# Optimization experiments

Measured on AMD Instinct MI355X. Metric: run time of the kernel, lower is better.

Reference implementation:

```python
import jax, jax.numpy as jnp
import numpy as np

N_NODES = 100000
N_EDGES = 3200000
IN_F, HID, OUT = 3, 32, 1
NEG_SLOPE = 0.2


def _glorot(key, shape):
    fan_in, fan_out = shape[0], shape[-1]
    lim = jnp.sqrt(6.0 / (fan_in + fan_out)).astype(jnp.float32)
    return jax.random.uniform(key, shape, jnp.float32, -lim, lim)


def setup_inputs() -> dict:
    key = jax.random.key(0)
    ks = jax.random.split(key, 12)
    x = jax.random.normal(ks[0], (N_NODES, IN_F), jnp.float32)
    edge_index = jax.random.randint(ks[1], (2, N_EDGES), 0, N_NODES, jnp.int32)
    return {
        "x": x,
        "edge_index": edge_index,
        "W1": _glorot(ks[2], (IN_F, HID)),
        "att_src1": _glorot(ks[3], (1, HID))[0],
        "att_dst1": _glorot(ks[4], (1, HID))[0],
        "b1": jnp.zeros((HID,), jnp.float32),
        "W2": _glorot(ks[5], (HID, HID)),
        "att_src2": _glorot(ks[6], (1, HID))[0],
        "att_dst2": _glorot(ks[7], (1, HID))[0],
        "b2": jnp.zeros((HID,), jnp.float32),
        "Wl": _glorot(ks[8], (HID, OUT)),
        "bl": jnp.zeros((OUT,), jnp.float32),
    }


def gat_layer(x, src, dst, W, att_src, att_dst, b):
    # h: [N, HID] dense transform
    h = x @ W
    # per-node attention halves (compute once per node, gather per edge)
    a_s = h @ att_src  # [N]
    a_d = h @ att_dst  # [N]
    logits = jax.nn.leaky_relu(a_s[src] + a_d[dst], NEG_SLOPE)  # [E+N]
    # segment-softmax over incoming edges of each dst node
    m = jax.ops.segment_max(logits, dst, num_segments=N_NODES)
    m = jnp.where(jnp.isfinite(m), m, 0.0)
    ex = jnp.exp(logits - m[dst])
    denom = jax.ops.segment_sum(ex, dst, num_segments=N_NODES)
    coef = ex / (denom[dst] + 1e-16)
    # weighted scatter-aggregate of source messages
    out = jax.ops.segment_sum(coef[:, None] * h[src], dst, num_segments=N_NODES)
    return out + b


def reference(x, edge_index, W1, att_src1, att_dst1, b1, W2, att_src2, att_dst2, b2, Wl, bl):
    # PyG GATConv default: add self-loops
    loops = jnp.arange(N_NODES, dtype=edge_index.dtype)
    src = jnp.concatenate([edge_index[0], loops])
    dst = jnp.concatenate([edge_index[1], loops])
    h = gat_layer(x, src, dst, W1, att_src1, att_dst1, b1)
    h = jax.nn.relu(h)  # dropout is identity in eval
    h = gat_layer(h, src, dst, W2, att_src2, att_dst2, b2)
    h = jax.nn.relu(h)
    return h @ Wl + bl
```

## Files before the change

### kernel.cpp

```cpp
#include <hip/hip_runtime.h>
#include <hip/hip_fp16.h>

#define HID 32
#define BN 132
#define NBPAD 768
#define BSTRIDE 5120
#define CHUNK 4096

__device__ __forceinline__ float lrelu(float x) { return x > 0.0f ? x : 0.2f * x; }

__global__ void k_transform1(const float* __restrict__ x,
                             const float* __restrict__ W1,
                             const float* __restrict__ att_src,
                             const float* __restrict__ att_dst,
                             __half* __restrict__ hh,
                             float* __restrict__ a_s,
                             float* __restrict__ a_d,
                             int* __restrict__ cursor,
                             int N)
{
    int tid = blockIdx.x * blockDim.x + threadIdx.x;
    if (tid < NBPAD) cursor[tid] = 0;
    int n = tid >> 5;
    int f = tid & 31;
    if (n >= N) return;
    float x0 = x[n * 3 + 0], x1 = x[n * 3 + 1], x2 = x[n * 3 + 2];
    float hv = x0 * W1[f] + x1 * W1[HID + f] + x2 * W1[2 * HID + f];
    hh[(size_t)n * HID + f] = __float2half(hv);
    float as = hv * att_src[f];
    float ad = hv * att_dst[f];
    #pragma unroll
    for (int m = 16; m >= 1; m >>= 1) {
        as += __shfl_xor(as, m, 32);
        ad += __shfl_xor(ad, m, 32);
    }
    if (f == 0) { a_s[n] = as; a_d[n] = ad; }
}

__global__ void __launch_bounds__(256) k_binscatter(const int* __restrict__ src,
                                                    const int* __restrict__ dst,
                                                    int* __restrict__ cursor,
                                                    unsigned int* __restrict__ packed,
                                                    int NBr, int E)
{
    __shared__ int stage[CHUNK];
    __shared__ unsigned short sbid[CHUNK];
    __shared__ int lhist[NBPAD], lexcl[NBPAD], lbase[NBPAD], lcur[NBPAD];
    __shared__ int arr[256];
    int t = threadIdx.x;
    for (int i = t; i < NBPAD; i += 256) { lhist[i] = 0; lcur[i] = 0; }
    __syncthreads();
    int base = blockIdx.x * CHUNK;
    int cnt = E - base; if (cnt > CHUNK) cnt = CHUNK;
    for (int i = t; i < cnt; i += 256)
        atomicAdd(&lhist[dst[base + i] / BN], 1);
    __syncthreads();
    int b0 = 3 * t;
    int c0 = lhist[b0], c1 = lhist[b0 + 1], c2 = lhist[b0 + 2];
    int s = c0 + c1 + c2;
    arr[t] = s;
    __syncthreads();
    for (int o = 1; o < 256; o <<= 1) {
        int v = (t >= o) ? arr[t - o] : 0;
        __syncthreads();
        arr[t] += v;
        __syncthreads();
    }
    int ex = arr[t] - s;
    int e0 = ex, e1 = ex + c0, e2 = ex + c0 + c1;
    lexcl[b0] = e0; lexcl[b0 + 1] = e1; lexcl[b0 + 2] = e2;
    for (int i = 0; i < c0; ++i) sbid[e0 + i] = (unsigned short)b0;
    for (int i = 0; i < c1; ++i) sbid[e1 + i] = (unsigned short)(b0 + 1);
    for (int i = 0; i < c2; ++i) sbid[e2 + i] = (unsigned short)(b0 + 2);
    for (int b = t; b < NBr; b += 256)
        if (lhist[b]) lbase[b] = b * BSTRIDE + atomicAdd(&cursor[b], lhist[b]);
    __syncthreads();
    for (int i = t; i < cnt; i += 256) {
        int d = dst[base + i];
        int sv = src[base + i];
        int b = d / BN;
        int dl = d - b * BN;
        int idx = lexcl[b] + atomicAdd(&lcur[b], 1);
        stage[idx] = (int)((unsigned)sv | ((unsigned)dl << 17));
    }
    __syncthreads();
    for (int i = t; i < cnt; i += 256) {
        int b = sbid[i];
        int gpos = lbase[b] + (i - lexcl[b]);
        if (gpos < (b + 1) * BSTRIDE)
            packed[gpos] = (unsigned)stage[i];
    }
}

__device__ __forceinline__ void agg_node(const __half* __restrict__ hh,
                                         const float* __restrict__ a_s,
                                         float a_dn, float a_sn,
                                         const float* __restrict__ b,
                                         int n, int f,
                                         const int* lcsr, int off, int dg,
                                         float& vx, float& vy)
{
    float ex = __expf(lrelu(a_sn + a_dn));
    float den = ex;
    float2 hs = __half22float2(*(const __half2*)(hh + (size_t)n * HID + 2 * f));
    float accx = ex * hs.x;
    float accy = ex * hs.y;
    for (int base = 0; base < dg; base += 16) {
        int m = dg - base; if (m > 16) m = 16;
        int sv = 0;
        float exv = 0.0f;
        if (f < m) {
            sv = lcsr[off + base + f];
            exv = __expf(lrelu(a_s[sv] + a_dn));
        }
        int j = 0;
        for (; j + 8 <= m; j += 8) {
            int s0 = __shfl(sv, j, 16), s1 = __shfl(sv, j + 1, 16);
            int s2 = __shfl(sv, j + 2, 16), s3 = __shfl(sv, j + 3, 16);
            int s4 = __shfl(sv, j + 4, 16), s5 = __shfl(sv, j + 5, 16);
            int s6 = __shfl(sv, j + 6, 16), s7 = __shfl(sv, j + 7, 16);
            float e0 = __shfl(exv, j, 16), e1 = __shfl(exv, j + 1, 16);
            float e2 = __shfl(exv, j + 2, 16), e3 = __shfl(exv, j + 3, 16);
            float e4 = __shfl(exv, j + 4, 16), e5 = __shfl(exv, j + 5, 16);
            float e6 = __shfl(exv, j + 6, 16), e7 = __shfl(exv, j + 7, 16);
            __half2 p0 = *(const __half2*)(hh + (size_t)s0 * HID + 2 * f);
            __half2 p1 = *(const __half2*)(hh + (size_t)s1 * HID + 2 * f);
            __half2 p2 = *(const __half2*)(hh + (size_t)s2 * HID + 2 * f);
            __half2 p3 = *(const __half2*)(hh + (size_t)s3 * HID + 2 * f);
            __half2 p4 = *(const __half2*)(hh + (size_t)s4 * HID + 2 * f);
            __half2 p5 = *(const __half2*)(hh + (size_t)s5 * HID + 2 * f);
            __half2 p6 = *(const __half2*)(hh + (size_t)s6 * HID + 2 * f);
            __half2 p7 = *(const __half2*)(hh + (size_t)s7 * HID + 2 * f);
            float2 q0 = __half22float2(p0), q1 = __half22float2(p1);
            float2 q2 = __half22float2(p2), q3 = __half22float2(p3);
            float2 q4 = __half22float2(p4), q5 = __half22float2(p5);
            float2 q6 = __half22float2(p6), q7 = __half22float2(p7);
            den += ((e0 + e1) + (e2 + e3)) + ((e4 + e5) + (e6 + e7));
            accx = fmaf(e0, q0.x, accx); accy = fmaf(e0, q0.y, accy);
            accx = fmaf(e1, q1.x, accx); accy = fmaf(e1, q1.y, accy);
            accx = fmaf(e2, q2.x, accx); accy = fmaf(e2, q2.y, accy);
            accx = fmaf(e3, q3.x, accx); accy = fmaf(e3, q3.y, accy);
            accx = fmaf(e4, q4.x, accx); accy = fmaf(e4, q4.y, accy);
            accx = fmaf(e5, q5.x, accx); accy = fmaf(e5, q5.y, accy);
            accx = fmaf(e6, q6.x, accx); accy = fmaf(e6, q6.y, accy);
            accx = fmaf(e7, q7.x, accx); accy = fmaf(e7, q7.y, accy);
        }
        for (; j + 4 <= m; j += 4) {
            int s0 = __shfl(sv, j, 16), s1 = __shfl(sv, j + 1, 16);
            int s2 = __shfl(sv, j + 2, 16), s3 = __shfl(sv, j + 3, 16);
            float e0 = __shfl(exv, j, 16), e1 = __shfl(exv, j + 1, 16);
            float e2 = __shfl(exv, j + 2, 16), e3 = __shfl(exv, j + 3, 16);
            __half2 p0 = *(const __half2*)(hh + (size_t)s0 * HID + 2 * f);
            __half2 p1 = *(const __half2*)(hh + (size_t)s1 * HID + 2 * f);
            __half2 p2 = *(const __half2*)(hh + (size_t)s2 * HID + 2 * f);
            __half2 p3 = *(const __half2*)(hh + (size_t)s3 * HID + 2 * f);
            float2 q0 = __half22float2(p0), q1 = __half22float2(p1);
            float2 q2 = __half22float2(p2), q3 = __half22float2(p3);
            den += (e0 + e1) + (e2 + e3);
            accx = fmaf(e0, q0.x, accx); accy = fmaf(e0, q0.y, accy);
            accx = fmaf(e1, q1.x, accx); accy = fmaf(e1, q1.y, accy);
            accx = fmaf(e2, q2.x, accx); accy = fmaf(e2, q2.y, accy);
            accx = fmaf(e3, q3.x, accx); accy = fmaf(e3, q3.y, accy);
        }
        for (; j < m; ++j) {
            int s0 = __shfl(sv, j, 16);
            float e0 = __shfl(exv, j, 16);
            float2 q0 = __half22float2(*(const __half2*)(hh + (size_t)s0 * HID + 2 * f));
            den += e0;
            accx = fmaf(e0, q0.x, accx);
            accy = fmaf(e0, q0.y, accy);
        }
    }
    float inv = 1.0f / (den + 1e-16f);
    vx = fmaxf(accx * inv + b[2 * f], 0.0f);
    vy = fmaxf(accy * inv + b[2 * f + 1], 0.0f);
}

__device__ __forceinline__ int build_lcsr(const unsigned int* pk, int cnt,
                                          int* lcsr, int* lhist, int* lscan, int* lcur)
{
    int t = threadIdx.x;
    if (t < 256) { lhist[t] = 0; lcur[t] = 0; }
    __syncthreads();
    for (int i = t; i < cnt; i += 512)
        atomicAdd(&lhist[(pk[i] >> 17) & 255], 1);
    __syncthreads();
    if (t < 256) lscan[t] = lhist[t];
    __syncthreads();
    for (int o = 1; o < 256; o <<= 1) {
        int v = (t < 256 && t >= o) ? lscan[t - o] : 0;
        __syncthreads();
        if (t < 256) lscan[t] += v;
        __syncthreads();
    }
    for (int i = t; i < cnt; i += 512) {
        unsigned int p = pk[i];
        int dl = (p >> 17) & 255;
        int pos = atomicAdd(&lcur[dl], 1);
        lcsr[(lscan[dl] - lhist[dl]) + pos] = (int)(p & 0x1FFFF);
    }
    __syncthreads();
    return cnt;
}

__global__ void __launch_bounds__(512) k_agg_mid_f(const __half* __restrict__ hh,
                          const float* __restrict__ a_s,
                          const float* __restrict__ a_d,
                          const int* __restrict__ cursor,
                          const unsigned int* __restrict__ packed,
                          const float* __restrict__ b1,
                          const float* __restrict__ W2,
                          const float* __restrict__ as2w,
                          const float* __restrict__ ad2w,
                          __half* __restrict__ hh_out,
                          float* __restrict__ as_out,
                          float* __restrict__ ad_out,
                          int N)
{
    __shared__ int lcsr[BSTRIDE];
    __shared__ int lhist[256], lscan[256], lcur[256];
    int bk = blockIdx.x, t = threadIdx.x;
    int cnt = cursor[bk]; if (cnt > BSTRIDE) cnt = BSTRIDE;
    build_lcsr(packed + (size_t)bk * BSTRIDE, cnt, lcsr, lhist, lscan, lcur);
    int g = t >> 4, f = t & 15;
    for (int dl = g; dl < BN; dl += 32) {
        int n = bk * BN + dl;
        if (n >= N) continue;
        int off = lscan[dl] - lhist[dl];
        int dg = lhist[dl];
        float vx, vy;
        agg_node(hh, a_s, a_d[n], a_s[n], b1, n, f, lcsr, off, dg, vx, vy);
        float hx = 0.0f, hy = 0.0f;
        #pragma unroll
        for (int k = 0; k < 16; ++k) {
            float va = __shfl(vx, k, 16);
            float vb = __shfl(vy, k, 16);
            float2 w0 = *(const float2*)(W2 + (2 * k) * HID + 2 * f);
            float2 w1 = *(const float2*)(W2 + (2 * k + 1) * HID + 2 * f);
            hx = fmaf(va, w0.x, hx); hy = fmaf(va, w0.y, hy);
            hx = fmaf(vb, w1.x, hx); hy = fmaf(vb, w1.y, hy);
        }
        *(__half2*)(hh_out + (size_t)n * HID + 2 * f) = __floats2half2_rn(hx, hy);
        float as = hx * as2w[2 * f] + hy * as2w[2 * f + 1];
        float ad = hx * ad2w[2 * f] + hy * ad2w[2 * f + 1];
        #pragma unroll
        for (int m2 = 8; m2 >= 1; m2 >>= 1) {
            as += __shfl_xor(as, m2, 16);
            ad += __shfl_xor(ad, m2, 16);
        }
        if (f == 0) { as_out[n] = as; ad_out[n] = ad; }
    }
}

__global__ void __launch_bounds__(512) k_agg_out_f(const __half* __restrict__ hh,
                          const float* __restrict__ a_s,
                          const float* __restrict__ a_d,
                          const int* __restrict__ cursor,
                          const unsigned int* __restrict__ packed,
                          const float* __restrict__ b2,
                          const float* __restrict__ Wl,
                          const float* __restrict__ bl,
                          float* __restrict__ out,
                          int N)
{
    __shared__ int lcsr[BSTRIDE];
    __shared__ int lhist[256], lscan[256], lcur[256];
    int bk = blockIdx.x, t = threadIdx.x;
    int cnt = cursor[bk]; if (cnt > BSTRIDE) cnt = BSTRIDE;
    build_lcsr(packed + (size_t)bk * BSTRIDE, cnt, lcsr, lhist, lscan, lcur);
    int g = t >> 4, f = t & 15;
    for (int dl = g; dl < BN; dl += 32) {
        int n = bk * BN + dl;
        if (n >= N) continue;
        int off = lscan[dl] - lhist[dl];
        int dg = lhist[dl];
        float vx, vy;
        agg_node(hh, a_s, a_d[n], a_s[n], b2, n, f, lcsr, off, dg, vx, vy);
        float y = vx * Wl[2 * f] + vy * Wl[2 * f + 1];
        #pragma unroll
        for (int m2 = 8; m2 >= 1; m2 >>= 1)
            y += __shfl_xor(y, m2, 16);
        if (f == 0) out[n] = y + bl[0];
    }
}

extern "C" void kernel_launch(void* const* d_in, const int* in_sizes, int n_in,
                              void* d_out, int out_size, void* d_ws, size_t ws_size,
                              hipStream_t stream)
{
    const float* x        = (const float*)d_in[0];
    const int*   eidx     = (const int*)d_in[1];
    const float* W1       = (const float*)d_in[2];
    const float* att_src1 = (const float*)d_in[3];
    const float* att_dst1 = (const float*)d_in[4];
    const float* b1       = (const float*)d_in[5];
    const float* W2       = (const float*)d_in[6];
    const float* att_src2 = (const float*)d_in[7];
    const float* att_dst2 = (const float*)d_in[8];
    const float* b2       = (const float*)d_in[9];
    const float* Wl       = (const float*)d_in[10];
    const float* bl       = (const float*)d_in[11];
    float* out = (float*)d_out;

    int N = in_sizes[0] / 3;
    int E = in_sizes[1] / 2;
    const int* src = eidx;
    const int* dst = eidx + E;
    int NBr = (N + BN - 1) / BN;

    size_t szNHh = (size_t)N * HID * 2;
    size_t szN4  = (size_t)N * 4;
    size_t szPK  = (size_t)NBr * BSTRIDE * 4;

    char* ws = (char*)d_ws;
    __half* h1h    = (__half*)ws; ws += szNHh;
    __half* h2h    = (__half*)ws; ws += szNHh;
    unsigned int* packed = (unsigned int*)ws; ws += szPK;
    float*  a_s1   = (float*)ws;  ws += szN4;
    float*  a_d1   = (float*)ws;  ws += szN4;
    float*  a_s2   = (float*)ws;  ws += szN4;
    float*  a_d2   = (float*)ws;  ws += szN4;
    int*    cursor = (int*)ws;    ws += NBPAD * 4;

    const int B = 256;
    int gridNode32 = (N * HID + B - 1) / B;
    int gridBin    = (E + CHUNK - 1) / CHUNK;

    k_transform1<<<gridNode32, B, 0, stream>>>(x, W1, att_src1, att_dst1,
                                               h1h, a_s1, a_d1, cursor, N);
    k_binscatter<<<gridBin, B, 0, stream>>>(src, dst, cursor, packed, NBr, E);
    k_agg_mid_f<<<NBr, 512, 0, stream>>>(h1h, a_s1, a_d1, cursor, packed,
                                         b1, W2, att_src2, att_dst2,
                                         h2h, a_s2, a_d2, N);
    k_agg_out_f<<<NBr, 512, 0, stream>>>(h2h, a_s2, a_d2, cursor, packed,
                                         b2, Wl, bl, out, N);
}
```

Baseline: 259.7 us.

## Aggregate each node with 8 lanes of 4 features using 8-byte gathers

The per-node aggregation group shrinks from 16 lanes handling 2 half features each to 8 lanes handling 4 features each. Each gather becomes an 8-byte load, and two nodes are processed per 16 lanes. Edges are consumed in batches of 8, with all loads issued before the FMAs. The W2 transform and reductions are reshaped to match. This aims to halve the gather instruction count and improve lane utilisation for low-degree nodes, at the cost of more registers and fewer edges batched per shuffle round.

```diff
diff --git a/kernel.cpp b/kernel.cpp
--- a/kernel.cpp
+++ b/kernel.cpp
@@ -92,92 +92,72 @@
     }
 }
 
-__device__ __forceinline__ void agg_node(const __half* __restrict__ hh,
-                                         const float* __restrict__ a_s,
-                                         float a_dn, float a_sn,
-                                         const float* __restrict__ b,
-                                         int n, int f,
-                                         const int* lcsr, int off, int dg,
-                                         float& vx, float& vy)
+__device__ __forceinline__ void agg_node8(const __half* __restrict__ hh,
+                                          const float* __restrict__ a_s,
+                                          float a_dn, float a_sn,
+                                          const float* __restrict__ b,
+                                          int n, int f,
+                                          const int* lcsr, int off, int dg,
+                                          float& v0, float& v1, float& v2, float& v3)
 {
     float ex = __expf(lrelu(a_sn + a_dn));
     float den = ex;
-    float2 hs = __half22float2(*(const __half2*)(hh + (size_t)n * HID + 2 * f));
-    float accx = ex * hs.x;
-    float accy = ex * hs.y;
-    for (int base = 0; base < dg; base += 16) {
-        int m = dg - base; if (m > 16) m = 16;
+    float2 sr = *(const float2*)(hh + (size_t)n * HID + 4 * f);
+    float2 s01 = __half22float2(*(__half2*)&sr.x);
+    float2 s23 = __half22float2(*(__half2*)&sr.y);
+    float a0 = ex * s01.x, a1 = ex * s01.y, a2 = ex * s23.x, a3 = ex * s23.y;
+    for (int base = 0; base < dg; base += 8) {
+        int m = dg - base; if (m > 8) m = 8;
         int sv = 0;
         float exv = 0.0f;
         if (f < m) {
             sv = lcsr[off + base + f];
             exv = __expf(lrelu(a_s[sv] + a_dn));
         }
-        int j = 0;
-        for (; j + 8 <= m; j += 8) {
-            int s0 = __shfl(sv, j, 16), s1 = __shfl(sv, j + 1, 16);
-            int s2 = __shfl(sv, j + 2, 16), s3 = __shfl(sv, j + 3, 16);
-            int s4 = __shfl(sv, j + 4, 16), s5 = __shfl(sv, j + 5, 16);
-            int s6 = __shfl(sv, j + 6, 16), s7 = __shfl(sv, j + 7, 16);
-            float e0 = __shfl(exv, j, 16), e1 = __shfl(exv, j + 1, 16);
-            float e2 = __shfl(exv, j + 2, 16), e3 = __shfl(exv, j + 3, 16);
-            float e4 = __shfl(exv, j + 4, 16), e5 = __shfl(exv, j + 5, 16);
-            float e6 = __shfl(exv, j + 6, 16), e7 = __shfl(exv, j + 7, 16);
-            __half2 p0 = *(const __half2*)(hh + (size_t)s0 * HID + 2 * f);
-            __half2 p1 = *(const __half2*)(hh + (size_t)s1 * HID + 2 * f);
-            __half2 p2 = *(const __half2*)(hh + (size_t)s2 * HID + 2 * f);
-            __half2 p3 = *(const __half2*)(hh + (size_t)s3 * HID + 2 * f);
-            __half2 p4 = *(const __half2*)(hh + (size_t)s4 * HID + 2 * f);
-            __half2 p5 = *(const __half2*)(hh + (size_t)s5 * HID + 2 * f);
-            __half2 p6 = *(const __half2*)(hh + (size_t)s6 * HID + 2 * f);
-            __half2 p7 = *(const __half2*)(hh + (size_t)s7 * HID + 2 * f);
-            float2 q0 = __half22float2(p0), q1 = __half22float2(p1);
-            float2 q2 = __half22float2(p2), q3 = __half22float2(p3);
-            float2 q4 = __half22float2(p4), q5 = __half22float2(p5);
-            float2 q6 = __half22float2(p6), q7 = __half22float2(p7);
-            den += ((e0 + e1) + (e2 + e3)) + ((e4 + e5) + (e6 + e7));
-            accx = fmaf(e0, q0.x, accx); accy = fmaf(e0, q0.y, accy);
-            accx = fmaf(e1, q1.x, accx); accy = fmaf(e1, q1.y, accy);
-            accx = fmaf(e2, q2.x, accx); accy = fmaf(e2, q2.y, accy);
-            accx = fmaf(e3, q3.x, accx); accy = fmaf(e3, q3.y, accy);
-            accx = fmaf(e4, q4.x, accx); accy = fmaf(e4, q4.y, accy);
-            accx = fmaf(e5, q5.x, accx); accy = fmaf(e5, q5.y, accy);
-            accx = fmaf(e6, q6.x, accx); accy = fmaf(e6, q6.y, accy);
-            accx = fmaf(e7, q7.x, accx); accy = fmaf(e7, q7.y, accy);
+        if (m == 8) {
+            int sA[8]; float eA[8]; float2 rA[8];
+            #pragma unroll
+            for (int j = 0; j < 8; ++j) {
+                sA[j] = __shfl(sv, j, 8);
+                eA[j] = __shfl(exv, j, 8);
+            }
+            #pragma unroll
+            for (int j = 0; j < 8; ++j)
+                rA[j] = *(const float2*)(hh + (size_t)sA[j] * HID + 4 * f);
+            #pragma unroll
+            for (int j = 0; j < 8; ++j) {
+                float2 q01 = __half22float2(*(__half2*)&rA[j].x);
+                float2 q23 = __half22float2(*(__half2*)&rA[j].y);
+                den += eA[j];
+                a0 = fmaf(eA[j], q01.x, a0);
+                a1 = fmaf(eA[j], q01.y, a1);
+                a2 = fmaf(eA[j], q23.x, a2);
+                a3 = fmaf(eA[j], q23.y, a3);
+            }
+        } else {
+            for (int j = 0; j < m; ++j) {
+                int s0 = __shfl(sv, j, 8);
+                float e0 = __shfl(exv, j, 8);
+                float2 r = *(const float2*)(hh + (size_t)s0 * HID + 4 * f);
+                float2 q01 = __half22float2(*(__half2*)&r.x);
+                float2 q23 = __half22float2(*(__half2*)&r.y);
+                den += e0;
+                a0 = fmaf(e0, q01.x, a0);
+                a1 = fmaf(e0, q01.y, a1);
+                a2 = fmaf(e0, q23.x, a2);
+                a3 = fmaf(e0, q23.y, a3);
+            }
         }
-        for (; j + 4 <= m; j += 4) {
-            int s0 = __shfl(sv, j, 16), s1 = __shfl(sv, j + 1, 16);
-            int s2 = __shfl(sv, j + 2, 16), s3 = __shfl(sv, j + 3, 16);
-            float e0 = __shfl(exv, j, 16), e1 = __shfl(exv, j + 1, 16);
-            float e2 = __shfl(exv, j + 2, 16), e3 = __shfl(exv, j + 3, 16);
-            __half2 p0 = *(const __half2*)(hh + (size_t)s0 * HID + 2 * f);
-            __half2 p1 = *(const __half2*)(hh + (size_t)s1 * HID + 2 * f);
-            __half2 p2 = *(const __half2*)(hh + (size_t)s2 * HID + 2 * f);
-            __half2 p3 = *(const __half2*)(hh + (size_t)s3 * HID + 2 * f);
-            float2 q0 = __half22float2(p0), q1 = __half22float2(p1);
-            float2 q2 = __half22float2(p2), q3 = __half22float2(p3);
-            den += (e0 + e1) + (e2 + e3);
-            accx = fmaf(e0, q0.x, accx); accy = fmaf(e0, q0.y, accy);
-            accx = fmaf(e1, q1.x, accx); accy = fmaf(e1, q1.y, accy);
-            accx = fmaf(e2, q2.x, accx); accy = fmaf(e2, q2.y, accy);
-            accx = fmaf(e3, q3.x, accx); accy = fmaf(e3, q3.y, accy);
-        }
-        for (; j < m; ++j) {
-            int s0 = __shfl(sv, j, 16);
-            float e0 = __shfl(exv, j, 16);
-            float2 q0 = __half22float2(*(const __half2*)(hh + (size_t)s0 * HID + 2 * f));
-            den += e0;
-            accx = fmaf(e0, q0.x, accx);
-            accy = fmaf(e0, q0.y, accy);
-        }
     }
     float inv = 1.0f / (den + 1e-16f);
-    vx = fmaxf(accx * inv + b[2 * f], 0.0f);
-    vy = fmaxf(accy * inv + b[2 * f + 1], 0.0f);
-}
-
-__device__ __forceinline__ int build_lcsr(const unsigned int* pk, int cnt,
-                                          int* lcsr, int* lhist, int* lscan, int* lcur)
+    v0 = fmaxf(a0 * inv + b[4 * f + 0], 0.0f);
+    v1 = fmaxf(a1 * inv + b[4 * f + 1], 0.0f);
+    v2 = fmaxf(a2 * inv + b[4 * f + 2], 0.0f);
+    v3 = fmaxf(a3 * inv + b[4 * f + 3], 0.0f);
+}
+
+__device__ __forceinline__ void build_lcsr(const unsigned int* pk, int cnt,
+                                           int* lcsr, int* lhist, int* lscan, int* lcur)
 {
     int t = threadIdx.x;
     if (t < 256) { lhist[t] = 0; lcur[t] = 0; }
@@ -200,7 +180,6 @@
         lcsr[(lscan[dl] - lhist[dl]) + pos] = (int)(p & 0x1FFFF);
     }
     __syncthreads();
-    return cnt;
 }
 
 __global__ void __launch_bounds__(512) k_agg_mid_f(const __half* __restrict__ hh,
@@ -222,31 +201,46 @@
     int bk = blockIdx.x, t = threadIdx.x;
     int cnt = cursor[bk]; if (cnt > BSTRIDE) cnt = BSTRIDE;
     build_lcsr(packed + (size_t)bk * BSTRIDE, cnt, lcsr, lhist, lscan, lcur);
-    int g = t >> 4, f = t & 15;
-    for (int dl = g; dl < BN; dl += 32) {
+    int g = t >> 3, f = t & 7;
+    for (int dl = g; dl < BN; dl += 64) {
         int n = bk * BN + dl;
         if (n >= N) continue;
         int off = lscan[dl] - lhist[dl];
         int dg = lhist[dl];
-        float vx, vy;
-        agg_node(hh, a_s, a_d[n], a_s[n], b1, n, f, lcsr, off, dg, vx, vy);
-        float hx = 0.0f, hy = 0.0f;
+        float v0, v1, v2, v3;
+        agg_node8(hh, a_s, a_d[n], a_s[n], b1, n, f, lcsr, off, dg, v0, v1, v2, v3);
+        float o0 = 0.0f, o1 = 0.0f, o2 = 0.0f, o3 = 0.0f;
         #pragma unroll
-        for (int k = 0; k < 16; ++k) {
-            float va = __shfl(vx, k, 16);
-            float vb = __shfl(vy, k, 16);
-            float2 w0 = *(const float2*)(W2 + (2 * k) * HID + 2 * f);
-            float2 w1 = *(const float2*)(W2 + (2 * k + 1) * HID + 2 * f);
-            hx = fmaf(va, w0.x, hx); hy = fmaf(va, w0.y, hy);
-            hx = fmaf(vb, w1.x, hx); hy = fmaf(vb, w1.y, hy);
+        for (int k = 0; k < 8; ++k) {
+            float bb0 = __shfl(v0, k, 8);
+            float bb1 = __shfl(v1, k, 8);
+            float bb2 = __shfl(v2, k, 8);
+            float bb3 = __shfl(v3, k, 8);
+            float4 w0 = *(const float4*)(W2 + (4 * k + 0) * HID + 4 * f);
+            float4 w1 = *(const float4*)(W2 + (4 * k + 1) * HID + 4 * f);
+            float4 w2 = *(const float4*)(W2 + (4 * k + 2) * HID + 4 * f);
+            float4 w3 = *(const float4*)(W2 + (4 * k + 3) * HID + 4 * f);
+            o0 = fmaf(bb0, w0.x, o0); o1 = fmaf(bb0, w0.y, o1);
+            o2 = fmaf(bb0, w0.z, o2); o3 = fmaf(bb0, w0.w, o3);
+            o0 = fmaf(bb1, w1.x, o0); o1 = fmaf(bb1, w1.y, o1);
+            o2 = fmaf(bb1, w1.z, o2); o3 = fmaf(bb1, w1.w, o3);
+            o0 = fmaf(bb2, w2.x, o0); o1 = fmaf(bb2, w2.y, o1);
+            o2 = fmaf(bb2, w2.z, o2); o3 = fmaf(bb2, w2.w, o3);
+            o0 = fmaf(bb3, w3.x, o0); o1 = fmaf(bb3, w3.y, o1);
+            o2 = fmaf(bb3, w3.z, o2); o3 = fmaf(bb3, w3.w, o3);
         }
-        *(__half2*)(hh_out + (size_t)n * HID + 2 * f) = __floats2half2_rn(hx, hy);
-        float as = hx * as2w[2 * f] + hy * as2w[2 * f + 1];
-        float ad = hx * ad2w[2 * f] + hy * ad2w[2 * f + 1];
+        float2 st;
+        *(__half2*)&st.x = __floats2half2_rn(o0, o1);
+        *(__half2*)&st.y = __floats2half2_rn(o2, o3);
+        *(float2*)(hh_out + (size_t)n * HID + 4 * f) = st;
+        float as = o0 * as2w[4 * f] + o1 * as2w[4 * f + 1]
+                 + o2 * as2w[4 * f + 2] + o3 * as2w[4 * f + 3];
+        float ad = o0 * ad2w[4 * f] + o1 * ad2w[4 * f + 1]
+                 + o2 * ad2w[4 * f + 2] + o3 * ad2w[4 * f + 3];
         #pragma unroll
-        for (int m2 = 8; m2 >= 1; m2 >>= 1) {
-            as += __shfl_xor(as, m2, 16);
-            ad += __shfl_xor(ad, m2, 16);
+        for (int m2 = 4; m2 >= 1; m2 >>= 1) {
+            as += __shfl_xor(as, m2, 8);
+            ad += __shfl_xor(ad, m2, 8);
         }
         if (f == 0) { as_out[n] = as; ad_out[n] = ad; }
     }
@@ -268,18 +262,19 @@
     int bk = blockIdx.x, t = threadIdx.x;
     int cnt = cursor[bk]; if (cnt > BSTRIDE) cnt = BSTRIDE;
     build_lcsr(packed + (size_t)bk * BSTRIDE, cnt, lcsr, lhist, lscan, lcur);
-    int g = t >> 4, f = t & 15;
-    for (int dl = g; dl < BN; dl += 32) {
+    int g = t >> 3, f = t & 7;
+    for (int dl = g; dl < BN; dl += 64) {
         int n = bk * BN + dl;
         if (n >= N) continue;
         int off = lscan[dl] - lhist[dl];
         int dg = lhist[dl];
-        float vx, vy;
-        agg_node(hh, a_s, a_d[n], a_s[n], b2, n, f, lcsr, off, dg, vx, vy);
-        float y = vx * Wl[2 * f] + vy * Wl[2 * f + 1];
+        float v0, v1, v2, v3;
+        agg_node8(hh, a_s, a_d[n], a_s[n], b2, n, f, lcsr, off, dg, v0, v1, v2, v3);
+        float y = v0 * Wl[4 * f] + v1 * Wl[4 * f + 1]
+                + v2 * Wl[4 * f + 2] + v3 * Wl[4 * f + 3];
         #pragma unroll
-        for (int m2 = 8; m2 >= 1; m2 >>= 1)
-            y += __shfl_xor(y, m2, 16);
+        for (int m2 = 4; m2 >= 1; m2 >>= 1)
+            y += __shfl_xor(y, m2, 8);
         if (f == 0) out[n] = y + bl[0];
     }
 }
```

After: 285.1 us. 1.1x slower.
